# Performance work log

Measured on AMD Instinct MI355X. Metric: run time of the kernel, lower is better.

Reference implementation:

```python
import jax, jax.numpy as jnp
import numpy as np

# Module constants (from init_kwargs / input_specs)
N = 192        # field size H == W
DX = 1.0       # pixel pitch
LAM = 0.5      # wavelength -> k = 2*pi/LAM
C = 2          # kernel oversize factor from the source
EPS = 1e-4


def _conv(a, w):
    # torch F.conv2d semantics: cross-correlation, VALID padding, stride 1.
    # a: [1,1,2N-1,2N-1] (physics kernel as conv input), w: [1,1,N,N] (field as weight)
    return jax.lax.conv_general_dilated(
        a, w, window_strides=(1, 1), padding='VALID',
        dimension_numbers=('NCHW', 'OIHW', 'NCHW'))


def _kernel_parts(z):
    # Rayleigh-Sommerfeld-like propagation kernel: K * (1/R) * exp(i*k*R)
    k = jnp.float32(2.0 * np.pi / LAM)
    n = jnp.arange(0.0, C * N * DX - 1.0, DX, dtype=jnp.float32)  # length 2N-1 (dx=1)
    X0 = jnp.float32(0.5 * DX * (C * N + EPS) - 1.0)              # Y0 == X0 (square)
    X = (n - X0)[:, None]
    Y = (n - X0)[None, :]
    r2 = X * X + Y * Y
    R = jnp.sqrt(r2 + z * z)
    RHO = jnp.sqrt(r2)
    Kfac = jnp.cos(jnp.arctan2(RHO, z))      # obliquity factor cos(theta)
    amp = Kfac / R
    ph = k * R
    # real / imag parts of K * kernel, shaped [1,1,2N-1,2N-1]
    return (amp * jnp.cos(ph))[None, None], (amp * jnp.sin(ph))[None, None]


def setup_inputs() -> dict:
    key = jax.random.key(0)
    k1, k2 = jax.random.split(key)
    return {
        'input_real': jax.random.normal(k1, (1, 1, N, N), dtype=jnp.float32),
        'input_imag': jax.random.normal(k2, (1, 1, N, N), dtype=jnp.float32),
        'z': jnp.ones((), dtype=jnp.float32) * 15.0,
    }


def reference(input_real, input_imag, z):
    Ar, Ai = _kernel_parts(z)
    # complex conv: (Ar + i*Ai) (*) (Fr + i*Fi)
    out_r = _conv(Ar, input_real) - _conv(Ai, input_imag)
    out_i = _conv(Ar, input_imag) + _conv(Ai, input_real)
    out = jax.lax.complex(out_r, out_i)
    # output.flip(-1, -2)
    return out[..., ::-1, ::-1]
```

## Files before the change

### kernel.cpp

```cpp
#include <hip/hip_runtime.h>

#define N 192
#define CCHUNK 8
#define NCHUNK 28
#define XT 39
#define XP 41

typedef __attribute__((ext_vector_type(8))) short short8;
typedef __attribute__((ext_vector_type(4))) float f32x4;

static __device__ __forceinline__ unsigned short f2bf(float x) {
    uint32_t u = __builtin_bit_cast(uint32_t, x);
    u += 0x7FFFu + ((u >> 16) & 1u);
    return (unsigned short)(u >> 16);
}

__global__ __launch_bounds__(256) void prep_kernel(const float* __restrict__ fr,
                                                   const float* __restrict__ fi,
                                                   const float* __restrict__ zp,
                                                   uint32_t* __restrict__ Abf,
                                                   uint32_t* __restrict__ Wt,
                                                   float* __restrict__ out) {
    int idx = blockIdx.x * 256 + threadIdx.x;
    float z = zp[0];
    if (idx < 384 * 384) {
        int r = idx / 384, c = idx - r * 384;
        uint32_t pack = 0u;
        if (r < 383 && c < 383) {
            const float X0 = 191.00005f;
            float xr = (float)r - X0;
            float yc = (float)c - X0;
            float r2 = xr * xr + yc * yc;
            float R2 = r2 + z * z;
            float R  = sqrtf(R2);
            float amp = z / R2;
            float ph = 12.566371f * R;
            float sv, cv;
            sincosf(ph, &sv, &cv);
            pack = (uint32_t)f2bf(amp * cv) | ((uint32_t)f2bf(-amp * sv) << 16);
        }
        Abf[idx] = pack;
    }
    if (idx < N * N) {
        int dy = idx / N, dx = idx - dy * N;
        Wt[dx * N + dy] = (uint32_t)f2bf(fr[idx]) | ((uint32_t)f2bf(fi[idx]) << 16);
        out[idx] = 0.f;
    }
}

__global__ __launch_bounds__(256) void s1_kernel(const uint32_t* __restrict__ Abf,
                                                 const uint32_t* __restrict__ Wt,
                                                 float* __restrict__ out) {
    __shared__ uint4 colAq[2][384];
    __shared__ float outT[64 * XP];

    const int tid  = threadIdx.x;
    const int l    = tid & 63;
    const int w    = tid >> 6;
    const int db   = blockIdx.x / NCHUNK;
    const int ck   = blockIdx.x - db * NCHUNK;
    const int ci0  = ck * CCHUNK;
    const int dx0  = db * 32;
    const int yoff = blockIdx.y * 64;
    const int m    = l & 15;
    const int kg   = l >> 4;

    uint4 bfr[2][12];
    #pragma unroll
    for (int t = 0; t < 2; ++t) {
        int dx = dx0 + t * 16 + m;
        #pragma unroll
        for (int ks = 0; ks < 12; ++ks)
            bfr[t][ks] = *(const uint4*)(Wt + dx * N + ks * 16 + kg * 4);
    }

    for (int e = tid; e < 64 * XP; e += 256) outT[e] = 0.f;

    {
        int c0 = dx0 + ci0;
        const uint32_t* ar = Abf + c0 * 384;
        for (int i = tid; i < 384; i += 256) {
            uint32_t e0 = ar[i];
            uint32_t e1 = (i < 383) ? ar[i + 1] : 0u;
            uint32_t e2 = (i < 382) ? ar[i + 2] : 0u;
            uint32_t e3 = (i < 381) ? ar[i + 3] : 0u;
            colAq[0][i] = make_uint4(e0, e1, e2, e3);
        }
    }
    __syncthreads();

    for (int q = 0; q < CCHUNK; ++q) {
        const int ci  = ci0 + q;
        const int cur = q & 1;
        if (q < CCHUNK - 1) {
            int cn = dx0 + ci + 1;
            const uint32_t* ar = Abf + cn * 384;
            for (int i = tid; i < 384; i += 256) {
                uint32_t e0 = ar[i];
                uint32_t e1 = (i < 383) ? ar[i + 1] : 0u;
                uint32_t e2 = (i < 382) ? ar[i + 2] : 0u;
                uint32_t e3 = (i < 381) ? ar[i + 3] : 0u;
                colAq[cur ^ 1][i] = make_uint4(e0, e1, e2, e3);
            }
        }

        f32x4 acc0 = {0.f, 0.f, 0.f, 0.f};
        f32x4 acc1 = {0.f, 0.f, 0.f, 0.f};
        const int srow = yoff + w * 16 + m;
        #pragma unroll
        for (int ks = 0; ks < 12; ++ks) {
            int s = srow + ks * 16 + kg * 4;
            uint4 aq = colAq[cur][s];
            union { uint4 q4; short8 v; } af, b0, b1;
            af.q4 = aq;
            b0.q4 = bfr[0][ks]; b1.q4 = bfr[1][ks];
            acc0 = __builtin_amdgcn_mfma_f32_16x16x32_bf16(af.v, b0.v, acc0, 0, 0, 0);
            acc1 = __builtin_amdgcn_mfma_f32_16x16x32_bf16(af.v, b1.v, acc1, 0, 0, 0);
        }

        if (ci < 223) {
            const int xb = q + 31;
            #pragma unroll
            for (int r = 0; r < 4; ++r) {
                int row = w * 16 + kg * 4 + r;
                outT[row * XP + xb - m]      += acc0[r];
                outT[row * XP + xb - 16 - m] += acc1[r];
            }
        }
        __syncthreads();
    }

    const int xg0 = ci0 - 31;
    for (int e = tid; e < 64 * XT; e += 256) {
        int row = e / XT, xt = e - row * XT;
        int x = xg0 + xt;
        if (x >= 0 && x < N) {
            int y = yoff + row;
            atomicAdd(&out[(191 - y) * N + (191 - x)], outT[row * XP + xt]);
        }
    }
}

extern "C" void kernel_launch(void* const* d_in, const int* in_sizes, int n_in,
                              void* d_out, int out_size, void* d_ws, size_t ws_size,
                              hipStream_t stream) {
    const float* fr = (const float*)d_in[0];
    const float* fi = (const float*)d_in[1];
    const float* zp = (const float*)d_in[2];

    uint32_t* Abf = (uint32_t*)d_ws;
    uint32_t* Wt  = Abf + 384 * 384;

    prep_kernel<<<576, 256, 0, stream>>>(fr, fi, zp, Abf, Wt, (float*)d_out);
    s1_kernel<<<dim3(6 * NCHUNK, 3), 256, 0, stream>>>(Abf, Wt, (float*)d_out);
}
```

Baseline: 29.62 us.

## Preload all chunk columns into LDS and drop per-step barriers

Loads all eight kernel columns for the chunk into shared memory in one pass with 16-byte loads. This replaces the double-buffered per-iteration prefetch and removes the barrier inside the q loop, leaving one barrier after the loop. It also adds a minimum-occupancy launch bound and empty asm statements to keep the weight fragments in registers. Shared memory per block grows to about 60KB, which limits how many blocks fit on a CU. The prefetch of the next column no longer overlaps with the MFMA work.

```diff
diff --git a/kernel.cpp b/kernel.cpp
--- a/kernel.cpp
+++ b/kernel.cpp
@@ -48,10 +48,10 @@
     }
 }
 
-__global__ __launch_bounds__(256) void s1_kernel(const uint32_t* __restrict__ Abf,
-                                                 const uint32_t* __restrict__ Wt,
-                                                 float* __restrict__ out) {
-    __shared__ uint4 colAq[2][384];
+__global__ __launch_bounds__(256, 2) void s1_kernel(const uint32_t* __restrict__ Abf,
+                                                    const uint32_t* __restrict__ Wt,
+                                                    float* __restrict__ out) {
+    __shared__ uint4 colAq[CCHUNK][384];
     __shared__ float outT[64 * XP];
 
     const int tid  = threadIdx.x;
@@ -70,47 +70,33 @@
     for (int t = 0; t < 2; ++t) {
         int dx = dx0 + t * 16 + m;
         #pragma unroll
-        for (int ks = 0; ks < 12; ++ks)
+        for (int ks = 0; ks < 12; ++ks) {
             bfr[t][ks] = *(const uint4*)(Wt + dx * N + ks * 16 + kg * 4);
+            asm volatile("" : "+v"(bfr[t][ks].x), "+v"(bfr[t][ks].y),
+                              "+v"(bfr[t][ks].z), "+v"(bfr[t][ks].w));
+        }
     }
 
     for (int e = tid; e < 64 * XP; e += 256) outT[e] = 0.f;
 
-    {
-        int c0 = dx0 + ci0;
-        const uint32_t* ar = Abf + c0 * 384;
-        for (int i = tid; i < 384; i += 256) {
-            uint32_t e0 = ar[i];
-            uint32_t e1 = (i < 383) ? ar[i + 1] : 0u;
-            uint32_t e2 = (i < 382) ? ar[i + 2] : 0u;
-            uint32_t e3 = (i < 381) ? ar[i + 3] : 0u;
-            colAq[0][i] = make_uint4(e0, e1, e2, e3);
-        }
+    for (int i = tid; i < CCHUNK * 384; i += 256) {
+        int j = i / 384, s = i - j * 384;
+        uint4 v;
+        __builtin_memcpy(&v, Abf + (dx0 + ci0 + j) * 384 + s, 16);
+        colAq[j][s] = v;
     }
     __syncthreads();
 
+    #pragma unroll 2
     for (int q = 0; q < CCHUNK; ++q) {
-        const int ci  = ci0 + q;
-        const int cur = q & 1;
-        if (q < CCHUNK - 1) {
-            int cn = dx0 + ci + 1;
-            const uint32_t* ar = Abf + cn * 384;
-            for (int i = tid; i < 384; i += 256) {
-                uint32_t e0 = ar[i];
-                uint32_t e1 = (i < 383) ? ar[i + 1] : 0u;
-                uint32_t e2 = (i < 382) ? ar[i + 2] : 0u;
-                uint32_t e3 = (i < 381) ? ar[i + 3] : 0u;
-                colAq[cur ^ 1][i] = make_uint4(e0, e1, e2, e3);
-            }
-        }
-
+        const int ci = ci0 + q;
         f32x4 acc0 = {0.f, 0.f, 0.f, 0.f};
         f32x4 acc1 = {0.f, 0.f, 0.f, 0.f};
         const int srow = yoff + w * 16 + m;
         #pragma unroll
         for (int ks = 0; ks < 12; ++ks) {
             int s = srow + ks * 16 + kg * 4;
-            uint4 aq = colAq[cur][s];
+            uint4 aq = colAq[q][s];
             union { uint4 q4; short8 v; } af, b0, b1;
             af.q4 = aq;
             b0.q4 = bfr[0][ks]; b1.q4 = bfr[1][ks];
@@ -127,8 +113,8 @@
                 outT[row * XP + xb - 16 - m] += acc1[r];
             }
         }
-        __syncthreads();
     }
+    __syncthreads();
 
     const int xg0 = ci0 - 31;
     for (int e = tid; e < 64 * XT; e += 256) {
```

Result: no change. 29.83 us (+0.7%).
